# Kernel tuning notes

Hardware: AMD Instinct MI355X
Metric: run time of the kernel (lower is better)

## Reference

```python
import jax, jax.numpy as jnp
import numpy as np

RADIUS = 3  # local window half-size -> K = (2*RADIUS+1)**2 = 49 taps


def _bilinear_sample_zeros(img_flat, x, y, h, w):
    """Bilinear sampling with zeros padding (grid_sample, align_corners=True).
    img_flat: (B, C, H*W); x, y: (P, K) pixel-space coords. Returns (B, C, P, K).
    align_corners=True denormalization exactly inverts the normalization in the
    original module, so we sample directly at pixel coordinates.
    """
    B, C, _ = img_flat.shape
    x0 = jnp.floor(x)
    y0 = jnp.floor(y)
    out = jnp.zeros((B, C) + x.shape, dtype=img_flat.dtype)
    corners = [
        (x0,       y0,       (x0 + 1 - x) * (y0 + 1 - y)),
        (x0 + 1.0, y0,       (x - x0) * (y0 + 1 - y)),
        (x0,       y0 + 1.0, (x0 + 1 - x) * (y - y0)),
        (x0 + 1.0, y0 + 1.0, (x - x0) * (y - y0)),
    ]
    for xi, yi, wt in corners:
        inb = (xi >= 0) & (xi < w) & (yi >= 0) & (yi < h)
        xi_c = jnp.clip(xi, 0, w - 1).astype(jnp.int32)
        yi_c = jnp.clip(yi, 0, h - 1).astype(jnp.int32)
        idx = (yi_c * w + xi_c).reshape(-1)            # (P*K,)
        v = jnp.take(img_flat, idx, axis=2)            # (B, C, P*K)
        v = v.reshape(B, C, *x.shape)                  # (B, C, P, K)
        out = out + v * (wt * inb.astype(img_flat.dtype))[None, None]
    return out


def reference(feature0, feature1):
    n, c, s, h, w = feature0.shape
    B = n * s
    f0 = feature0.transpose(0, 2, 1, 3, 4).reshape(B, c, h, w)
    f1 = feature1.transpose(0, 2, 1, 3, 4).reshape(B, c, h, w)

    r = RADIUS
    # base pixel coords (x, y), flattened row-major over (h, w) -> (P, 2)
    yy, xx = jnp.meshgrid(jnp.arange(h, dtype=jnp.float32),
                          jnp.arange(w, dtype=jnp.float32), indexing='ij')
    base = jnp.stack([xx, yy], axis=-1).reshape(h * w, 2)  # (P, 2)

    # window offsets (dx, dy), dy outer / dx inner ordering -> (K, 2)
    dys, dxs = jnp.meshgrid(jnp.arange(-r, r + 1, dtype=jnp.float32),
                            jnp.arange(-r, r + 1, dtype=jnp.float32), indexing='ij')
    offs = jnp.stack([dxs, dys], axis=-1).reshape(-1, 2)   # (K, 2)

    sample = base[:, None, :] + offs[None, :, :]           # (P, K, 2)
    valid = ((sample[..., 0] >= 0) & (sample[..., 0] < w) &
             (sample[..., 1] >= 0) & (sample[..., 1] < h))  # (P, K)

    f1_flat = f1.reshape(B, c, h * w)
    wf = _bilinear_sample_zeros(f1_flat, sample[..., 0], sample[..., 1], h, w)  # (B, c, P, K)

    f0_flat = f0.reshape(B, c, h * w)
    corr = jnp.einsum('bcp,bcpk->bpk', f0_flat, wf) / jnp.asarray(c, jnp.float32) ** 0.5
    corr = jnp.where(valid[None], corr, -jnp.inf)
    prob = jax.nn.softmax(corr, axis=-1)                   # (B, P, K)

    corresp = jnp.einsum('bpk,pkj->bpj', prob, sample)     # (B, P, 2) expected (x, y)
    flow = corresp - base[None]                            # (B, P, 2)
    flow = flow.reshape(n, s, h, w, 2).transpose(0, 4, 1, 2, 3)  # (n, 2, s, h, w)
    return flow


def setup_inputs() -> dict:
    key = jax.random.key(0)
    k0, k1 = jax.random.split(key)
    n, c, s, h, w = 2, 64, 4, 64, 44
    feature0 = jax.random.normal(k0, (n, c, s, h, w), dtype=jnp.float32)
    feature1 = jax.random.normal(k1, (n, c, s, h, w), dtype=jnp.float32)
    return {"feature0": feature0, "feature1": feature1}
```

## Files before the change

### kernel.cpp

```cpp
#include <hip/hip_runtime.h>
#include <math.h>

#define N_  2
#define C_  64
#define S_  4
#define H_  64
#define W_  44
#define HW_       (H_ * W_)
#define CH_STRIDE (S_ * HW_)
#define NSTRIDE   (C_ * S_ * HW_)

typedef _Float16 h8 __attribute__((ext_vector_type(8)));
typedef float    f4 __attribute__((ext_vector_type(4)));

__global__ __launch_bounds__(448) void flow_kernel(
    const float* __restrict__ f0,
    const float* __restrict__ f1,
    float* __restrict__ out)
{
    const int lane = threadIdx.x & 63;
    const int w    = threadIdx.x >> 6;
    const int b    = blockIdx.x & 7;
    const int y    = blockIdx.x >> 3;
    const int n_idx = b >> 2;
    const int s_idx = b & 3;
    const int base  = n_idx * NSTRIDE + s_idx * HW_;

    __shared__ float corr[W_][49];

    const int row = y + w - 3;
    if (row >= 0 && row < H_) {
        const int quad = lane >> 4;
        const int l16  = lane & 15;

        h8 afr[3][2];
        #pragma unroll
        for (int mi = 0; mi < 3; ++mi) {
            const int  x  = mi * 16 + l16;
            const bool av = (x < W_);
            const float* pa = f0 + base + y * W_ + (av ? x : 0);
            #pragma unroll
            for (int kh = 0; kh < 2; ++kh) {
                const int ch0 = (kh * 4 + quad) * 8;
                float v[8];
                #pragma unroll
                for (int j = 0; j < 8; ++j)
                    v[j] = pa[(size_t)(ch0 + j) * CH_STRIDE];
                h8 a;
                #pragma unroll
                for (int j = 0; j < 8; ++j)
                    a[j] = av ? (_Float16)v[j] : (_Float16)0.0f;
                afr[mi][kh] = a;
            }
        }

        const float* pb_row = f1 + base + row * W_;
        f4 acc[3][2];
        #pragma unroll
        for (int mi = 0; mi < 3; ++mi) {
            #pragma unroll
            for (int nh = 0; nh < 2; ++nh) {
                const int  col = mi * 16 + nh * 16 - 8 + l16;
                const bool bv  = (col >= 0) && (col < W_);
                const float* pb = pb_row + (bv ? col : 0);
                f4 a = {0.f, 0.f, 0.f, 0.f};
                #pragma unroll
                for (int kh = 0; kh < 2; ++kh) {
                    const int ch0 = (kh * 4 + quad) * 8;
                    float v[8];
                    #pragma unroll
                    for (int j = 0; j < 8; ++j)
                        v[j] = pb[(size_t)(ch0 + j) * CH_STRIDE];
                    h8 bf;
                    #pragma unroll
                    for (int j = 0; j < 8; ++j)
                        bf[j] = bv ? (_Float16)v[j] : (_Float16)0.0f;
                    a = __builtin_amdgcn_mfma_f32_16x16x32_f16(
                            afr[mi][kh], bf, a, 0, 0, 0);
                }
                acc[mi][nh] = a;
            }
        }

        #pragma unroll
        for (int mi = 0; mi < 3; ++mi) {
            #pragma unroll
            for (int nh = 0; nh < 2; ++nh) {
                #pragma unroll
                for (int r = 0; r < 4; ++r) {
                    const int x   = mi * 16 + quad * 4 + r;
                    const int col = mi * 16 + nh * 16 - 8 + l16;
                    const int dx  = col - x + 3;
                    if (x < W_ && dx >= 0 && dx < 7)
                        corr[x][w * 7 + dx] = acc[mi][nh][r] * 0.125f;
                }
            }
        }
    }

    __syncthreads();

    if (w == 0) {
        const int xe = min(lane, W_ - 1);
        float c[49];
        float m = -1e30f;
        #pragma unroll
        for (int k = 0; k < 49; ++k) {
            const int kdy = k / 7, kdx = k % 7;
            const int col = lane + kdx - 3;
            const int rr  = y + kdy - 3;
            const bool ok = (col >= 0) && (col < W_) && (rr >= 0) && (rr < H_);
            const float v = ok ? corr[xe][k] : -1e30f;
            c[k] = v;
            m = fmaxf(m, v);
        }
        float S = 0.0f, Sx = 0.0f, Sy = 0.0f;
        #pragma unroll
        for (int k = 0; k < 49; ++k) {
            const float e = __expf(c[k] - m);
            S  += e;
            Sx += e * (float)(k % 7 - 3);
            Sy += e * (float)(k / 7 - 3);
        }
        if (lane < W_) {
            const float inv = 1.0f / S;
            const int ob = (n_idx * 2) * S_ * HW_ + s_idx * HW_ + y * W_ + lane;
            out[ob]            = Sx * inv;
            out[ob + S_ * HW_] = Sy * inv;
        }
    }
}

extern "C" void kernel_launch(void* const* d_in, const int* in_sizes, int n_in,
                              void* d_out, int out_size, void* d_ws, size_t ws_size,
                              hipStream_t stream) {
    const float* f0 = (const float*)d_in[0];
    const float* f1 = (const float*)d_in[1];
    float* out = (float*)d_out;

    flow_kernel<<<8 * H_, 448, 0, stream>>>(f0, f1, out);
}
```

Measured before the change: 68.74 us.

## Stage f0/f1 rows into fp16 LDS slabs before MFMA correlation

Each of the seven row warps now loads its full f1 row once (64 channels, with halo) into shared memory as fp16, and a new eighth warp loads the f0 row into a separate fp16 slab. The MFMA loop then reads its A and B fragments from LDS instead of issuing strided global loads per fragment, which previously re-fetched overlapping f1 columns across the mi/nh tiles. This adds a barrier and about 64KB of shared memory per block, which may reduce occupancy, and each thread holds 64 floats in registers during the load.

```diff
diff --git a/kernel.cpp b/kernel.cpp
--- a/kernel.cpp
+++ b/kernel.cpp
@@ -13,70 +13,92 @@
 typedef _Float16 h8 __attribute__((ext_vector_type(8)));
 typedef float    f4 __attribute__((ext_vector_type(4)));
 
-__global__ __launch_bounds__(448) void flow_kernel(
+__global__ __launch_bounds__(512) void flow_kernel(
     const float* __restrict__ f0,
     const float* __restrict__ f1,
     float* __restrict__ out)
 {
     const int lane = threadIdx.x & 63;
     const int w    = threadIdx.x >> 6;
-    const int b    = blockIdx.x & 7;
-    const int y    = blockIdx.x >> 3;
+
+    const int b = blockIdx.x & 7;
+    const int y = blockIdx.x >> 3;
     const int n_idx = b >> 2;
     const int s_idx = b & 3;
     const int base  = n_idx * NSTRIDE + s_idx * HW_;
 
+    __shared__ __align__(16) _Float16 slabF1[7 * 8 * 64 * 8];
+    __shared__ __align__(16) _Float16 slabF0[8 * 48 * 8];
     __shared__ float corr[W_][49];
 
-    const int row = y + w - 3;
-    if (row >= 0 && row < H_) {
+    const int row     = y + w - 3;
+    const bool row_ok = (row >= 0) && (row < H_);
+
+    if (w < 7) {
+        if (row_ok) {
+            const int col   = lane - 8;
+            const bool vld  = (col >= 0) && (col < W_);
+            const int cc    = min(max(col, 0), W_ - 1);
+            const float* p  = f1 + base + row * W_ + cc;
+            float v[64];
+            #pragma unroll
+            for (int j = 0; j < 64; ++j)
+                v[j] = p[(size_t)j * CH_STRIDE];
+            #pragma unroll
+            for (int c8 = 0; c8 < 8; ++c8) {
+                h8 pk;
+                #pragma unroll
+                for (int j = 0; j < 8; ++j)
+                    pk[j] = vld ? (_Float16)v[c8 * 8 + j] : (_Float16)0.0f;
+                *(h8*)&slabF1[((w * 8 + c8) * 64 + lane) * 8] = pk;
+            }
+        }
+    } else {
+        if (lane < 48) {
+            const bool vld = (lane < W_);
+            const int  xc  = min(lane, W_ - 1);
+            const float* p = f0 + base + y * W_ + xc;
+            float v[64];
+            #pragma unroll
+            for (int j = 0; j < 64; ++j)
+                v[j] = p[(size_t)j * CH_STRIDE];
+            #pragma unroll
+            for (int c8 = 0; c8 < 8; ++c8) {
+                h8 pk;
+                #pragma unroll
+                for (int j = 0; j < 8; ++j)
+                    pk[j] = vld ? (_Float16)v[c8 * 8 + j] : (_Float16)0.0f;
+                *(h8*)&slabF0[(c8 * 48 + lane) * 8] = pk;
+            }
+        }
+    }
+
+    __syncthreads();
+
+    if (w < 7 && row_ok) {
         const int quad = lane >> 4;
         const int l16  = lane & 15;
 
         h8 afr[3][2];
         #pragma unroll
-        for (int mi = 0; mi < 3; ++mi) {
-            const int  x  = mi * 16 + l16;
-            const bool av = (x < W_);
-            const float* pa = f0 + base + y * W_ + (av ? x : 0);
+        for (int mi = 0; mi < 3; ++mi)
             #pragma unroll
-            for (int kh = 0; kh < 2; ++kh) {
-                const int ch0 = (kh * 4 + quad) * 8;
-                float v[8];
-                #pragma unroll
-                for (int j = 0; j < 8; ++j)
-                    v[j] = pa[(size_t)(ch0 + j) * CH_STRIDE];
-                h8 a;
-                #pragma unroll
-                for (int j = 0; j < 8; ++j)
-                    a[j] = av ? (_Float16)v[j] : (_Float16)0.0f;
-                afr[mi][kh] = a;
-            }
-        }
+            for (int kh = 0; kh < 2; ++kh)
+                afr[mi][kh] = *(const h8*)
+                    &slabF0[((kh * 4 + quad) * 48 + (mi * 16 + l16)) * 8];
 
-        const float* pb_row = f1 + base + row * W_;
+        const _Float16* myslab = &slabF1[w * (8 * 64 * 8)];
         f4 acc[3][2];
         #pragma unroll
         for (int mi = 0; mi < 3; ++mi) {
             #pragma unroll
             for (int nh = 0; nh < 2; ++nh) {
-                const int  col = mi * 16 + nh * 16 - 8 + l16;
-                const bool bv  = (col >= 0) && (col < W_);
-                const float* pb = pb_row + (bv ? col : 0);
                 f4 a = {0.f, 0.f, 0.f, 0.f};
                 #pragma unroll
                 for (int kh = 0; kh < 2; ++kh) {
-                    const int ch0 = (kh * 4 + quad) * 8;
-                    float v[8];
-                    #pragma unroll
-                    for (int j = 0; j < 8; ++j)
-                        v[j] = pb[(size_t)(ch0 + j) * CH_STRIDE];
-                    h8 bf;
-                    #pragma unroll
-                    for (int j = 0; j < 8; ++j)
-                        bf[j] = bv ? (_Float16)v[j] : (_Float16)0.0f;
-                    a = __builtin_amdgcn_mfma_f32_16x16x32_f16(
-                            afr[mi][kh], bf, a, 0, 0, 0);
+                    const h8 bfr = *(const h8*)
+                        &myslab[((kh * 4 + quad) * 64 + (mi * 16 + nh * 16 + l16)) * 8];
+                    a = __builtin_amdgcn_mfma_f32_16x16x32_f16(afr[mi][kh], bfr, a, 0, 0, 0);
                 }
                 acc[mi][nh] = a;
             }
@@ -138,5 +160,5 @@
     const float* f1 = (const float*)d_in[1];
     float* out = (float*)d_out;
 
-    flow_kernel<<<8 * H_, 448, 0, stream>>>(f0, f1, out);
+    flow_kernel<<<8 * H_, 512, 0, stream>>>(f0, f1, out);
 }
```

Result: faster. 65.50 us (-4.7%).
